# Kernel optimization log

Measured on AMD Instinct MI355X. Metric: run time of the kernel, lower is better.

## Reference

```python
import jax, jax.numpy as jnp
import numpy as np

EPS = 1e-5


def _gcn_norm(edge_index, N):
    # symmetric GCN normalization with self-loops: D^-1/2 (A+I) D^-1/2
    row, col = edge_index[0], edge_index[1]
    loop = jnp.arange(N, dtype=row.dtype)
    row_f = jnp.concatenate([row, loop])
    col_f = jnp.concatenate([col, loop])
    deg = jax.ops.segment_sum(jnp.ones_like(row_f, dtype=jnp.float32), row_f, num_segments=N)
    dinv = jnp.where(deg > 0, jax.lax.rsqrt(jnp.maximum(deg, 1.0)), 0.0)
    norm = dinv[row_f] * dinv[col_f]  # [E+N]
    return row_f, col_f, norm


def _gcn_conv(h, W, b, row_f, col_f, norm, N):
    h = h @ W  # [N, C_out] small GEMM
    msg = h[col_f] * norm[:, None]  # gather over edges  [E+N, C_out]
    return jax.ops.segment_sum(msg, row_f, num_segments=N) + b


def _bn_eval(h, gamma, beta, mean, var):
    return (h - mean) * jax.lax.rsqrt(var + EPS) * gamma + beta


def setup_inputs() -> dict:
    key = jax.random.key(0)
    ks = jax.random.split(key, 12)
    N, E = 100000, 1600000
    C_in, C_hid, C_out = 64, 64, 64
    x = jax.random.normal(ks[0], (N, C_in), dtype=jnp.float32)
    edge_index = jax.random.randint(ks[1], (2, E), 0, N, dtype=jnp.int32)
    s = 1.0 / np.sqrt(C_hid)
    inp = {
        "x": x,
        "edge_index": edge_index,
        "W1": jax.random.normal(ks[2], (C_in, C_hid), dtype=jnp.float32) * s,
        "b1": jnp.zeros((C_hid,), jnp.float32),
        "g1": jnp.ones((C_hid,), jnp.float32),
        "be1": jnp.zeros((C_hid,), jnp.float32),
        "m1": jax.random.normal(ks[3], (C_hid,), dtype=jnp.float32) * 0.1,
        "v1": jax.random.uniform(ks[4], (C_hid,), minval=0.5, maxval=1.5, dtype=jnp.float32),
        "W2": jax.random.normal(ks[5], (C_hid, C_hid), dtype=jnp.float32) * s,
        "b2": jnp.zeros((C_hid,), jnp.float32),
        "g2": jnp.ones((C_hid,), jnp.float32),
        "be2": jnp.zeros((C_hid,), jnp.float32),
        "m2": jax.random.normal(ks[6], (C_hid,), dtype=jnp.float32) * 0.1,
        "v2": jax.random.uniform(ks[7], (C_hid,), minval=0.5, maxval=1.5, dtype=jnp.float32),
        "W3": jax.random.normal(ks[8], (C_hid, C_out), dtype=jnp.float32) * s,
        "b3": jnp.zeros((C_out,), jnp.float32),
    }
    return inp


def reference(x, edge_index, W1, b1, g1, be1, m1, v1, W2, b2, g2, be2, m2, v2, W3, b3):
    N = x.shape[0]
    row_f, col_f, norm = _gcn_norm(edge_index, N)  # cached=True: computed once
    h = _gcn_conv(x, W1, b1, row_f, col_f, norm, N)
    h = jax.nn.relu(_bn_eval(h, g1, be1, m1, v1))  # dropout off (eval)
    h = _gcn_conv(h, W2, b2, row_f, col_f, norm, N)
    h = jax.nn.relu(_bn_eval(h, g2, be2, m2, v2))
    global_embeddings = h
    hc_predictions = _gcn_conv(global_embeddings, W3, b3, row_f, col_f, norm, N)
    return (global_embeddings, hc_predictions)
```

## Files before the change

kernel.cpp:

```cpp
#include <hip/hip_runtime.h>

typedef __attribute__((ext_vector_type(8))) short bfrag8;
typedef __attribute__((ext_vector_type(4))) float facc4;
typedef __attribute__((ext_vector_type(8))) unsigned short u16x8;

#define CROWS  256
#define NCBMAX 512
#define CAP    8192
#define CHUNK  4096
#define SLACK  772
#define BPITCH (CAP + SLACK)

static __device__ __forceinline__ float bf2f(ushort u) {
    union { unsigned int i; float f; } x;
    x.i = ((unsigned int)u) << 16;
    return x.f;
}
static __device__ __forceinline__ ushort f2bf(float f) {
    union { float f; unsigned int i; } x;
    x.f = f;
    unsigned int r = x.i + 0x7FFFu + ((x.i >> 16) & 1u);
    return (ushort)(r >> 16);
}


__global__ void k_cinit(int* __restrict__ ccur, int ncb, ushort* __restrict__ t, int N) {
    int b = blockIdx.x * blockDim.x + threadIdx.x;
    if (b < ncb) ccur[b] = b * CAP;
    if (blockIdx.x == 0 && threadIdx.x < 64) t[(size_t)N * 64 + threadIdx.x] = 0;
}

__global__ void k_part(const int* __restrict__ row, const int* __restrict__ col, int E,
                       int* __restrict__ ccur, int* __restrict__ bkt, int ncb) {
    __shared__ int recs[CHUNK];
    __shared__ unsigned short cbl[CHUNK];
    __shared__ int hist[NCBMAX], lbase[NCBMAX], loff[NCBMAX];
    int tid = threadIdx.x;
    int chunk0 = blockIdx.x * CHUNK;
    for (int i = tid; i < ncb; i += blockDim.x) hist[i] = 0;
    __syncthreads();
    for (int j = tid; j < CHUNK; j += blockDim.x) {
        int e = chunk0 + j;
        if (e < E) {
            int r = row[e];
            int cb = r >> 8;
            recs[j] = ((r & (CROWS - 1)) << 17) | col[e];
            cbl[j] = (unsigned short)cb;
            atomicAdd(&hist[cb], 1);
        } else cbl[j] = 0xFFFF;
    }
    __syncthreads();
    for (int i = tid; i < ncb; i += blockDim.x) {
        int h = hist[i];
        lbase[i] = h ? atomicAdd(&ccur[i], h) : 0;
        loff[i] = 0;
    }
    __syncthreads();
    for (int j = tid; j < CHUNK; j += blockDim.x) {
        unsigned short cb = cbl[j];
        if (cb != 0xFFFF) {
            int p = lbase[cb] + atomicAdd(&loff[cb], 1);
            if (p < (cb + 1) * CAP) bkt[p] = recs[j];
        }
    }
}

__global__ void k_build(const int* __restrict__ bkt, const int* __restrict__ ccur,
                        int* __restrict__ rptr, int* __restrict__ deg,
                        float* __restrict__ dinv, int* __restrict__ cidx, int N) {
    __shared__ int hist[CROWS], wstart[CROWS], cur[CROWS], psum[CROWS];
    int tid = threadIdx.x;
    int b = blockIdx.x;
    int lo = b * CROWS;
    int nr = min(CROWS, N - lo);
    int in0 = b * CAP;
    int cntE = min(ccur[b] - in0, CAP);
    int out0 = b * BPITCH;

    if (tid < CROWS) hist[tid] = 0;
    __syncthreads();
    for (int i = tid; i < cntE; i += blockDim.x)
        atomicAdd(&hist[bkt[in0 + i] >> 17], 1);
    __syncthreads();
    int d = 0, ep = 0;
    if (tid < CROWS) {
        d = hist[tid];
        ep = (d + 3) & ~3;
        psum[tid] = ep;
    }
    __syncthreads();
    #pragma unroll
    for (int off = 1; off < CROWS; off <<= 1) {
        int t = (tid >= off && tid < CROWS) ? psum[tid - off] : 0;
        __syncthreads();
        if (tid < CROWS) psum[tid] += t;
        __syncthreads();
    }
    if (tid < CROWS) {
        int ws = out0 + psum[tid] - ep;
        wstart[tid] = ws;
        cur[tid] = ws;
        if (tid < nr) {
            rptr[lo + tid] = ws;
            deg[lo + tid] = d;
            dinv[lo + tid] = rsqrtf((float)(d + 1));
        }
    }
    __syncthreads();
    for (int i = tid; i < cntE; i += blockDim.x) {
        int v = bkt[in0 + i];
        int p = atomicAdd(&cur[v >> 17], 1);
        cidx[p] = v & 0x1FFFF;
    }
    __syncthreads();
    if (tid < nr)
        for (int j = d; j < ep; j++) cidx[wstart[tid] + j] = N;
}

template <bool FP32IN>
__global__ void k_gemm(const void* __restrict__ Hv, const float* __restrict__ W,
                       const float* __restrict__ dinv,
                       ushort* __restrict__ T, int ntiles, int N) {
    int lane = threadIdx.x & 63;
    int wid = (blockIdx.x * blockDim.x + threadIdx.x) >> 6;
    int nw = (gridDim.x * blockDim.x) >> 6;
    int m = lane & 15, quad = lane >> 4;

    bfrag8 bf[2][4];
    #pragma unroll
    for (int s = 0; s < 2; s++)
        #pragma unroll
        for (int c = 0; c < 4; c++) {
            bfrag8 f;
            #pragma unroll
            for (int j = 0; j < 8; j++) {
                int k = 32 * s + quad * 8 + j;
                f[j] = (short)f2bf(W[k * 64 + 16 * c + m]);
            }
            bf[s][c] = f;
        }

    for (int t = wid; t < ntiles; t += nw) {
        int nodeA = t * 16 + m;
        if (nodeA >= N) nodeA = N - 1;
        bfrag8 a0, a1;
        if (FP32IN) {
            const float* arow = (const float*)Hv + (size_t)nodeA * 64;
            #pragma unroll
            for (int s = 0; s < 2; s++) {
                float4 u0 = *(const float4*)(arow + s * 32 + quad * 8);
                float4 u1 = *(const float4*)(arow + s * 32 + quad * 8 + 4);
                bfrag8 f;
                f[0] = (short)f2bf(u0.x); f[1] = (short)f2bf(u0.y);
                f[2] = (short)f2bf(u0.z); f[3] = (short)f2bf(u0.w);
                f[4] = (short)f2bf(u1.x); f[5] = (short)f2bf(u1.y);
                f[6] = (short)f2bf(u1.z); f[7] = (short)f2bf(u1.w);
                if (s == 0) a0 = f; else a1 = f;
            }
        } else {
            const ushort* arow = (const ushort*)Hv + (size_t)nodeA * 64;
            a0 = *(const bfrag8*)(arow + quad * 8);
            a1 = *(const bfrag8*)(arow + 32 + quad * 8);
        }
        facc4 acc[4];
        #pragma unroll
        for (int c = 0; c < 4; c++) { acc[c][0]=0.f; acc[c][1]=0.f; acc[c][2]=0.f; acc[c][3]=0.f; }
        #pragma unroll
        for (int c = 0; c < 4; c++) {
            acc[c] = __builtin_amdgcn_mfma_f32_16x16x32_bf16(a0, bf[0][c], acc[c], 0, 0, 0);
            acc[c] = __builtin_amdgcn_mfma_f32_16x16x32_bf16(a1, bf[1][c], acc[c], 0, 0, 0);
        }
        #pragma unroll
        for (int c = 0; c < 4; c++)
            #pragma unroll
            for (int r = 0; r < 4; r++) {
                int node = t * 16 + quad * 4 + r;
                if (node < N)
                    T[(size_t)node * 64 + c * 16 + m] = f2bf(dinv[node] * acc[c][r]);
            }
    }
}

__global__ void k_agg(const ushort* __restrict__ T2, const int* __restrict__ rptr,
                      const int* __restrict__ deg, const float* __restrict__ dinv,
                      const int* __restrict__ cidx,
                      const float* __restrict__ bias, const float* __restrict__ g,
                      const float* __restrict__ be, const float* __restrict__ mm,
                      const float* __restrict__ vv, int do_bn,
                      float* __restrict__ outf, ushort* __restrict__ outb, int N) {
    int lane = threadIdx.x & 63;
    int wid = (blockIdx.x * blockDim.x + threadIdx.x) >> 6;
    int nw = (gridDim.x * blockDim.x) >> 6;
    int grp = lane >> 3;
    int s = lane & 7;

    float bb[8], sc[8], sh[8];
    #pragma unroll
    for (int k = 0; k < 8; k++) { bb[k] = bias[s * 8 + k]; sc[k] = 1.f; sh[k] = 0.f; }
    if (do_bn) {
        #pragma unroll
        for (int k = 0; k < 8; k++) {
            sc[k] = g[s * 8 + k] * rsqrtf(vv[s * 8 + k] + 1e-5f);
            sh[k] = be[s * 8 + k] - mm[s * 8 + k] * sc[k];
        }
    }

    int noct = (N + 7) >> 3;
    for (int q = wid; q < noct; q += nw) {
        int r = q * 8 + grp;
        bool rv = (r < N);
        int start = rv ? rptr[r] : 0;
        int ep = rv ? ((deg[r] + 3) & ~3) : 0;
        float a[8];
        #pragma unroll
        for (int k = 0; k < 8; k++) a[k] = 0.f;
        for (int i = 0; i < ep; i += 4) {
            int4 c4 = *(const int4*)(cidx + start + i);
            u16x8 t0 = *(const u16x8*)(T2 + (size_t)c4.x * 64 + s * 8);
            u16x8 t1 = *(const u16x8*)(T2 + (size_t)c4.y * 64 + s * 8);
            u16x8 t2 = *(const u16x8*)(T2 + (size_t)c4.z * 64 + s * 8);
            u16x8 t3 = *(const u16x8*)(T2 + (size_t)c4.w * 64 + s * 8);
            #pragma unroll
            for (int k = 0; k < 8; k++)
                a[k] += (bf2f(t0[k]) + bf2f(t1[k])) + (bf2f(t2[k]) + bf2f(t3[k]));
        }
        if (rv) {
            u16x8 sf = *(const u16x8*)(T2 + (size_t)r * 64 + s * 8);
            float dr = dinv[r];
            float v[8];
            #pragma unroll
            for (int k = 0; k < 8; k++) {
                v[k] = dr * (a[k] + bf2f(sf[k])) + bb[k];
                if (do_bn) v[k] = fmaxf(v[k] * sc[k] + sh[k], 0.f);
            }
            if (outf) {
                *(float4*)(outf + (size_t)r * 64 + s * 8) = make_float4(v[0], v[1], v[2], v[3]);
                *(float4*)(outf + (size_t)r * 64 + s * 8 + 4) = make_float4(v[4], v[5], v[6], v[7]);
            }
            if (outb) {
                u16x8 o;
                #pragma unroll
                for (int k = 0; k < 8; k++) o[k] = f2bf(v[k]);
                *(u16x8*)(outb + (size_t)r * 64 + s * 8) = o;
            }
        }
    }
}


extern "C" void kernel_launch(void* const* d_in, const int* in_sizes, int n_in,
                              void* d_out, int out_size, void* d_ws, size_t ws_size,
                              hipStream_t stream) {
    const float* x  = (const float*)d_in[0];
    const int*   ei = (const int*)d_in[1];
    const float *W1 = (const float*)d_in[2],  *b1 = (const float*)d_in[3];
    const float *g1 = (const float*)d_in[4],  *be1= (const float*)d_in[5];
    const float *m1 = (const float*)d_in[6],  *v1 = (const float*)d_in[7];
    const float *W2 = (const float*)d_in[8],  *b2 = (const float*)d_in[9];
    const float *g2 = (const float*)d_in[10], *be2= (const float*)d_in[11];
    const float *m2 = (const float*)d_in[12], *v2 = (const float*)d_in[13];
    const float *W3 = (const float*)d_in[14], *b3 = (const float*)d_in[15];

    int N = in_sizes[0] / 64;
    int E = in_sizes[1] / 2;
    const int* row = ei;
    const int* col = ei + E;
    int ncb = (N + CROWS - 1) / CROWS;

    char* p = (char*)d_ws;
    auto take = [&](size_t b) -> char* {
        char* q = p;
        p += (b + 255) & ~(size_t)255;
        return q;
    };
    int*    ccur  = (int*)   take((size_t)ncb * 4);
    int*    rptr  = (int*)   take((size_t)N * 4);
    int*    deg   = (int*)   take((size_t)N * 4);
    float*  dinv  = (float*) take((size_t)N * 4);
    int*    bkt   = (int*)   take((size_t)ncb * CAP * 4);
    int*    cidx  = (int*)   take((size_t)ncb * BPITCH * 4 + 1024);
    ushort* t     = (ushort*)take((size_t)(N + 1) * 64 * 2);
    ushort* h     = (ushort*)take((size_t)N * 64 * 2);

    const int TB = 256;
    const int TBP = 1024;
    int nchunks = (E + CHUNK - 1) / CHUNK;
    k_cinit<<<(ncb + TB - 1) / TB, TB, 0, stream>>>(ccur, ncb, t, N);
    k_part <<<nchunks, TBP, 0, stream>>>(row, col, E, ccur, bkt, ncb);
    k_build<<<ncb, TBP, 0, stream>>>(bkt, ccur, rptr, deg, dinv, cidx, N);

    float* outp = (float*)d_out;
    int ntiles = (N + 15) >> 4;
    int GG = (ntiles + 3) / 4;
    int noct = (N + 7) >> 3;
    int GA = (noct + 3) / 4;

    k_gemm<true> <<<GG, TB, 0, stream>>>(x, W1, dinv, t, ntiles, N);
    k_agg <<<GA, TB, 0, stream>>>(t, rptr, deg, dinv, cidx, b1, g1, be1, m1, v1, 1,
                                  (float*)nullptr, h, N);
    k_gemm<false><<<GG, TB, 0, stream>>>(h, W2, dinv, t, ntiles, N);
    k_agg <<<GA, TB, 0, stream>>>(t, rptr, deg, dinv, cidx, b2, g2, be2, m2, v2, 1,
                                  outp, h, N);
    k_gemm<false><<<GG, TB, 0, stream>>>(h, W3, dinv, t, ntiles, N);
    k_agg <<<GA, TB, 0, stream>>>(t, rptr, deg, dinv, cidx, b3, b3, b3, b3, b3, 0,
                                  outp + (size_t)N * 64, (ushort*)nullptr, N);
}
```

Before: 283.0 us.

## Fuse next-layer GEMM into aggregation epilogue and unroll gather by eight

The aggregation kernel now optionally runs the next layer's 64x64 GEMM in its epilogue. It stages each 32-row tile of the BN+ReLU output in LDS, multiplies it by the next weight matrix with MFMA, and writes dinv-scaled bf16 rows straight into a ping-pong T buffer. This removes two standalone GEMM launches and the write and reread of the intermediate h array. The edge gather loop is also unrolled to eight neighbours per iteration to raise memory-level parallelism. In exchange, the grid becomes one row per 8-lane group with no grid-stride loop, and every block reconverts the weights to bf16 from global memory.

```diff
diff --git a/kernel.cpp b/kernel.cpp
--- a/kernel.cpp
+++ b/kernel.cpp
@@ -24,10 +24,14 @@
 }
 
 
-__global__ void k_cinit(int* __restrict__ ccur, int ncb, ushort* __restrict__ t, int N) {
+__global__ void k_cinit(int* __restrict__ ccur, int ncb,
+                        ushort* __restrict__ ta, ushort* __restrict__ tb, int N) {
     int b = blockIdx.x * blockDim.x + threadIdx.x;
     if (b < ncb) ccur[b] = b * CAP;
-    if (blockIdx.x == 0 && threadIdx.x < 64) t[(size_t)N * 64 + threadIdx.x] = 0;
+    if (blockIdx.x == 0 && threadIdx.x < 64) {
+        ta[(size_t)N * 64 + threadIdx.x] = 0;
+        tb[(size_t)N * 64 + threadIdx.x] = 0;
+    }
 }
 
 __global__ void k_part(const int* __restrict__ row, const int* __restrict__ col, int E,
@@ -181,18 +185,25 @@
     }
 }
 
-__global__ void k_agg(const ushort* __restrict__ T2, const int* __restrict__ rptr,
-                      const int* __restrict__ deg, const float* __restrict__ dinv,
-                      const int* __restrict__ cidx,
-                      const float* __restrict__ bias, const float* __restrict__ g,
-                      const float* __restrict__ be, const float* __restrict__ mm,
-                      const float* __restrict__ vv, int do_bn,
-                      float* __restrict__ outf, ushort* __restrict__ outb, int N) {
-    int lane = threadIdx.x & 63;
-    int wid = (blockIdx.x * blockDim.x + threadIdx.x) >> 6;
-    int nw = (gridDim.x * blockDim.x) >> 6;
+template <bool FUSE>
+__global__ void k_aggf(const ushort* __restrict__ T2, const int* __restrict__ rptr,
+                       const int* __restrict__ deg, const float* __restrict__ dinv,
+                       const int* __restrict__ cidx,
+                       const float* __restrict__ bias, const float* __restrict__ g,
+                       const float* __restrict__ be, const float* __restrict__ mm,
+                       const float* __restrict__ vv, int do_bn,
+                       const float* __restrict__ Wn,
+                       float* __restrict__ outf, ushort* __restrict__ Tn, int N) {
+    __shared__ ushort lds_h[32][72];
+
+    int tid = threadIdx.x;
+    int lane = tid & 63;
+    int wl = tid >> 6;
     int grp = lane >> 3;
     int s = lane & 7;
+    int loc = wl * 8 + grp;
+    int r = blockIdx.x * 32 + loc;
+    bool rv = (r < N);
 
     float bb[8], sc[8], sh[8];
     #pragma unroll
@@ -205,45 +216,99 @@
         }
     }
 
-    int noct = (N + 7) >> 3;
-    for (int q = wid; q < noct; q += nw) {
-        int r = q * 8 + grp;
-        bool rv = (r < N);
-        int start = rv ? rptr[r] : 0;
-        int ep = rv ? ((deg[r] + 3) & ~3) : 0;
-        float a[8];
-        #pragma unroll
-        for (int k = 0; k < 8; k++) a[k] = 0.f;
-        for (int i = 0; i < ep; i += 4) {
-            int4 c4 = *(const int4*)(cidx + start + i);
-            u16x8 t0 = *(const u16x8*)(T2 + (size_t)c4.x * 64 + s * 8);
-            u16x8 t1 = *(const u16x8*)(T2 + (size_t)c4.y * 64 + s * 8);
-            u16x8 t2 = *(const u16x8*)(T2 + (size_t)c4.z * 64 + s * 8);
-            u16x8 t3 = *(const u16x8*)(T2 + (size_t)c4.w * 64 + s * 8);
-            #pragma unroll
-            for (int k = 0; k < 8; k++)
-                a[k] += (bf2f(t0[k]) + bf2f(t1[k])) + (bf2f(t2[k]) + bf2f(t3[k]));
-        }
-        if (rv) {
-            u16x8 sf = *(const u16x8*)(T2 + (size_t)r * 64 + s * 8);
-            float dr = dinv[r];
-            float v[8];
-            #pragma unroll
-            for (int k = 0; k < 8; k++) {
-                v[k] = dr * (a[k] + bf2f(sf[k])) + bb[k];
-                if (do_bn) v[k] = fmaxf(v[k] * sc[k] + sh[k], 0.f);
-            }
-            if (outf) {
-                *(float4*)(outf + (size_t)r * 64 + s * 8) = make_float4(v[0], v[1], v[2], v[3]);
-                *(float4*)(outf + (size_t)r * 64 + s * 8 + 4) = make_float4(v[4], v[5], v[6], v[7]);
-            }
-            if (outb) {
-                u16x8 o;
+    int start = rv ? rptr[r] : 0;
+    int ep = rv ? ((deg[r] + 3) & ~3) : 0;
+    float a[8];
+    #pragma unroll
+    for (int k = 0; k < 8; k++) a[k] = 0.f;
+    int i = 0;
+    for (; i + 8 <= ep; i += 8) {
+        int4 c4 = *(const int4*)(cidx + start + i);
+        int4 d4 = *(const int4*)(cidx + start + i + 4);
+        u16x8 t0 = *(const u16x8*)(T2 + (size_t)c4.x * 64 + s * 8);
+        u16x8 t1 = *(const u16x8*)(T2 + (size_t)c4.y * 64 + s * 8);
+        u16x8 t2 = *(const u16x8*)(T2 + (size_t)c4.z * 64 + s * 8);
+        u16x8 t3 = *(const u16x8*)(T2 + (size_t)c4.w * 64 + s * 8);
+        u16x8 t4 = *(const u16x8*)(T2 + (size_t)d4.x * 64 + s * 8);
+        u16x8 t5 = *(const u16x8*)(T2 + (size_t)d4.y * 64 + s * 8);
+        u16x8 t6 = *(const u16x8*)(T2 + (size_t)d4.z * 64 + s * 8);
+        u16x8 t7 = *(const u16x8*)(T2 + (size_t)d4.w * 64 + s * 8);
+        #pragma unroll
+        for (int k = 0; k < 8; k++)
+            a[k] += ((bf2f(t0[k]) + bf2f(t1[k])) + (bf2f(t2[k]) + bf2f(t3[k]))) +
+                    ((bf2f(t4[k]) + bf2f(t5[k])) + (bf2f(t6[k]) + bf2f(t7[k])));
+    }
+    if (i < ep) {
+        int4 c4 = *(const int4*)(cidx + start + i);
+        u16x8 t0 = *(const u16x8*)(T2 + (size_t)c4.x * 64 + s * 8);
+        u16x8 t1 = *(const u16x8*)(T2 + (size_t)c4.y * 64 + s * 8);
+        u16x8 t2 = *(const u16x8*)(T2 + (size_t)c4.z * 64 + s * 8);
+        u16x8 t3 = *(const u16x8*)(T2 + (size_t)c4.w * 64 + s * 8);
+        #pragma unroll
+        for (int k = 0; k < 8; k++)
+            a[k] += (bf2f(t0[k]) + bf2f(t1[k])) + (bf2f(t2[k]) + bf2f(t3[k]));
+    }
+
+    float v[8];
+    #pragma unroll
+    for (int k = 0; k < 8; k++) v[k] = 0.f;
+    if (rv) {
+        u16x8 sf = *(const u16x8*)(T2 + (size_t)r * 64 + s * 8);
+        float dr = dinv[r];
+        #pragma unroll
+        for (int k = 0; k < 8; k++) {
+            v[k] = dr * (a[k] + bf2f(sf[k])) + bb[k];
+            if (do_bn) v[k] = fmaxf(v[k] * sc[k] + sh[k], 0.f);
+        }
+        if (outf) {
+            *(float4*)(outf + (size_t)r * 64 + s * 8) = make_float4(v[0], v[1], v[2], v[3]);
+            *(float4*)(outf + (size_t)r * 64 + s * 8 + 4) = make_float4(v[4], v[5], v[6], v[7]);
+        }
+    }
+
+    if constexpr (FUSE) {
+        u16x8 hv;
+        #pragma unroll
+        for (int k = 0; k < 8; k++) hv[k] = rv ? f2bf(v[k]) : (ushort)0;
+        *(u16x8*)&lds_h[loc][s * 8] = hv;
+
+        int m = lane & 15, quad = lane >> 4;
+        int rtile = wl >> 1, chalf = wl & 1;
+        bfrag8 bw[2][2];
+        #pragma unroll
+        for (int ks = 0; ks < 2; ks++)
+            #pragma unroll
+            for (int c = 0; c < 2; c++) {
+                bfrag8 f;
                 #pragma unroll
-                for (int k = 0; k < 8; k++) o[k] = f2bf(v[k]);
-                *(u16x8*)(outb + (size_t)r * 64 + s * 8) = o;
-            }
-        }
+                for (int j = 0; j < 8; j++) {
+                    int k = 32 * ks + quad * 8 + j;
+                    f[j] = (short)f2bf(Wn[k * 64 + chalf * 32 + c * 16 + m]);
+                }
+                bw[ks][c] = f;
+            }
+        __syncthreads();
+
+        bfrag8 a0 = *(const bfrag8*)&lds_h[rtile * 16 + m][quad * 8];
+        bfrag8 a1 = *(const bfrag8*)&lds_h[rtile * 16 + m][32 + quad * 8];
+        facc4 acc[2];
+        #pragma unroll
+        for (int c = 0; c < 2; c++) { acc[c][0]=0.f; acc[c][1]=0.f; acc[c][2]=0.f; acc[c][3]=0.f; }
+        #pragma unroll
+        for (int c = 0; c < 2; c++) {
+            acc[c] = __builtin_amdgcn_mfma_f32_16x16x32_bf16(a0, bw[0][c], acc[c], 0, 0, 0);
+            acc[c] = __builtin_amdgcn_mfma_f32_16x16x32_bf16(a1, bw[1][c], acc[c], 0, 0, 0);
+        }
+        int nodeBase = blockIdx.x * 32 + rtile * 16;
+        #pragma unroll
+        for (int c = 0; c < 2; c++)
+            #pragma unroll
+            for (int rr = 0; rr < 4; rr++) {
+                int node = nodeBase + quad * 4 + rr;
+                if (node < N)
+                    Tn[(size_t)node * 64 + chalf * 32 + c * 16 + m] =
+                        f2bf(dinv[node] * acc[c][rr]);
+            }
     }
 }
 
@@ -279,29 +344,27 @@
     float*  dinv  = (float*) take((size_t)N * 4);
     int*    bkt   = (int*)   take((size_t)ncb * CAP * 4);
     int*    cidx  = (int*)   take((size_t)ncb * BPITCH * 4 + 1024);
-    ushort* t     = (ushort*)take((size_t)(N + 1) * 64 * 2);
-    ushort* h     = (ushort*)take((size_t)N * 64 * 2);
+    ushort* ta    = (ushort*)take((size_t)(N + 1) * 64 * 2);
+    ushort* tb    = (ushort*)take((size_t)(N + 1) * 64 * 2);
 
     const int TB = 256;
     const int TBP = 1024;
     int nchunks = (E + CHUNK - 1) / CHUNK;
-    k_cinit<<<(ncb + TB - 1) / TB, TB, 0, stream>>>(ccur, ncb, t, N);
+    k_cinit<<<(ncb + TB - 1) / TB, TB, 0, stream>>>(ccur, ncb, ta, tb, N);
     k_part <<<nchunks, TBP, 0, stream>>>(row, col, E, ccur, bkt, ncb);
     k_build<<<ncb, TBP, 0, stream>>>(bkt, ccur, rptr, deg, dinv, cidx, N);
 
     float* outp = (float*)d_out;
     int ntiles = (N + 15) >> 4;
     int GG = (ntiles + 3) / 4;
-    int noct = (N + 7) >> 3;
-    int GA = (noct + 3) / 4;
-
-    k_gemm<true> <<<GG, TB, 0, stream>>>(x, W1, dinv, t, ntiles, N);
-    k_agg <<<GA, TB, 0, stream>>>(t, rptr, deg, dinv, cidx, b1, g1, be1, m1, v1, 1,
-                                  (float*)nullptr, h, N);
-    k_gemm<false><<<GG, TB, 0, stream>>>(h, W2, dinv, t, ntiles, N);
-    k_agg <<<GA, TB, 0, stream>>>(t, rptr, deg, dinv, cidx, b2, g2, be2, m2, v2, 1,
-                                  outp, h, N);
-    k_gemm<false><<<GG, TB, 0, stream>>>(h, W3, dinv, t, ntiles, N);
-    k_agg <<<GA, TB, 0, stream>>>(t, rptr, deg, dinv, cidx, b3, b3, b3, b3, b3, 0,
-                                  outp + (size_t)N * 64, (ushort*)nullptr, N);
-}
+    int GA = (N + 31) / 32;
+
+    k_gemm<true><<<GG, TB, 0, stream>>>(x, W1, dinv, ta, ntiles, N);
+    k_aggf<true><<<GA, TB, 0, stream>>>(ta, rptr, deg, dinv, cidx, b1, g1, be1, m1, v1, 1,
+                                        W2, (float*)nullptr, tb, N);
+    k_aggf<true><<<GA, TB, 0, stream>>>(tb, rptr, deg, dinv, cidx, b2, g2, be2, m2, v2, 1,
+                                        W3, outp, ta, N);
+    k_aggf<false><<<GA, TB, 0, stream>>>(ta, rptr, deg, dinv, cidx, b3, b3, b3, b3, b3, 0,
+                                         (const float*)nullptr,
+                                         outp + (size_t)N * 64, (ushort*)nullptr, N);
+}
```

New measurement: 272.1 us. 3.9% less time.
